# Kernel optimization log

Hardware: AMD Instinct MI355X
Metric: run time of the kernel (lower is better)

## Reference

```python
import jax, jax.numpy as jnp
import numpy as np

MASK_OUT_VALUE = -10000.0


def setup_inputs() -> dict:
    key = jax.random.key(0)
    k1, k2, k3 = jax.random.split(key, 3)
    B, H, S, D = 2, 16, 2048, 64
    query = jax.random.normal(k1, (B, H, S, D), dtype=jnp.float32)
    key_t = jax.random.normal(k2, (B, H, S, D), dtype=jnp.float32)
    value = jax.random.normal(k3, (B, H, S, D), dtype=jnp.float32)
    # causal mask: (1, 1, S, S), True where attention is allowed
    mask = jnp.tril(jnp.ones((S, S), dtype=bool))[None, None, :, :]
    return {"query": query, "key": key_t, "value": value, "mask": mask}


def reference(query, key, value, mask):
    # scores: (B, H, S, S)
    scale = 1.0 / jnp.sqrt(jnp.asarray(query.shape[-1], query.dtype))
    attn_scores = jnp.einsum("bhqd,bhkd->bhqk", query, key) * scale
    attn_scores = jnp.where(mask, attn_scores,
                            jnp.asarray(MASK_OUT_VALUE, attn_scores.dtype))
    attn_weights = jax.nn.softmax(attn_scores, axis=-1)
    # dropout is identity (p=0 / eval mode)
    attn_output = jnp.einsum("bhqk,bhkd->bhqd", attn_weights, value)
    return attn_output
```

## Files before the change

kernel.cpp:

```cpp
#include <hip/hip_runtime.h>
#include <math.h>


#define S_LEN   2048
#define D_HEAD  64
#define SCALE_L2E 0.18033688011112042f
#define FIXM    8.0f

using bf16x8 = __attribute__((ext_vector_type(8))) short;
using f32x4  = __attribute__((ext_vector_type(4))) float;
using uint4v = __attribute__((ext_vector_type(4))) unsigned int;

__device__ __forceinline__ unsigned int rnd_bf(float f) {
  return __float_as_uint(f) + 0x8000u;
}
__device__ __forceinline__ unsigned short f2bf(float f) {
  return (unsigned short)(rnd_bf(f) >> 16);
}

__device__ __forceinline__ void gl_lds16(const unsigned short* g, unsigned short* l) {
  __builtin_amdgcn_global_load_lds(
      (const __attribute__((address_space(1))) unsigned int*)g,
      (__attribute__((address_space(3))) unsigned int*)l, 16, 0, 0);
}

__device__ __forceinline__ unsigned int cvtpk_bf16(float lo, float hi) {
  unsigned int r;
  asm("v_cvt_pk_bf16_f32 %0, %1, %2" : "=v"(r) : "v"(lo), "v"(hi));
  return r;
}
__device__ __forceinline__ void swap32(unsigned int& a, unsigned int& b) {
  asm("v_permlane32_swap_b32 %0, %1" : "+v"(a), "+v"(b));
}
__device__ __forceinline__ void swap16(unsigned int& a, unsigned int& b) {
  asm("v_permlane16_swap_b32 %0, %1" : "+v"(a), "+v"(b));
}

template <int CTRL>
__device__ __forceinline__ float dppf(float x) {
  return __builtin_bit_cast(float,
      __builtin_amdgcn_update_dpp(0, __builtin_bit_cast(int, x), CTRL, 0xF, 0xF, false));
}
__device__ __forceinline__ float rowsum16(float x) {
  x += dppf<0xB1>(x);
  x += dppf<0x4E>(x);
  x += dppf<0x124>(x);
  x += dppf<0x128>(x);
  return x;
}

__global__ __launch_bounds__(256, 4)
void prep(const float* __restrict__ Kg, const float* __restrict__ Vg,
          unsigned short* __restrict__ Kb, unsigned short* __restrict__ Vt)
{
  __shared__ __align__(16) unsigned short Lt[64][72];
  const int j = blockIdx.x, t = threadIdx.x;
  const int bh = j >> 4, seg = j & 15;
  const size_t base = (size_t)bh * (S_LEN * D_HEAD) + (size_t)seg * 128 * D_HEAD;
#pragma unroll
  for (int i = 0; i < 8; ++i) {
    const size_t idx = base + i * 1024 + t * 4;
    const f32x4 v = *(const f32x4*)(Kg + idx);
    uint2 pk;
    pk.x = (rnd_bf(v[1]) & 0xFFFF0000u) | (rnd_bf(v[0]) >> 16);
    pk.y = (rnd_bf(v[3]) & 0xFFFF0000u) | (rnd_bf(v[2]) >> 16);
    *(uint2*)(Kb + idx) = pk;
  }
  for (int h = 0; h < 2; ++h) {
    const int s0 = seg * 128 + h * 64;
    __syncthreads();
#pragma unroll
    for (int pp = 0; pp < 4; ++pp) {
      const int r = t >> 2;
      const int d0 = (t & 3) * 4 + pp * 16;
      const f32x4 v = *(const f32x4*)(Vg + (size_t)bh * (S_LEN * D_HEAD)
                                         + (size_t)(s0 + r) * D_HEAD + d0);
#pragma unroll
      for (int e = 0; e < 4; ++e) Lt[d0 + e][r] = f2bf(v[e]);
    }
    __syncthreads();
#pragma unroll
    for (int q = 0; q < 2; ++q) {
      const int d = t >> 2, ch = (t & 3) + 4 * q;
      *(uint4*)(Vt + (size_t)(bh * 64 + d) * S_LEN + s0 + ch * 8) =
          *(const uint4*)&Lt[d][ch * 8];
    }
  }
}

__global__ __launch_bounds__(256, 2)
void fa(const float* __restrict__ Qg, const unsigned short* __restrict__ Kb,
        const unsigned short* __restrict__ Vt, float* __restrict__ Og)
{
  __shared__ unsigned short Ks[2][64][64];
  __shared__ unsigned short Vs[2][64][64];

  const int id = blockIdx.x;
  const int bh = id & 31;
  const int pr = id >> 5;

  const int t    = threadIdx.x;
  const int w    = t >> 6;
  const int lane = t & 63;
  const int c    = lane & 15;
  const int quad = lane >> 4;

  const float* __restrict__ Qb = Qg + (size_t)bh * (S_LEN * D_HEAD);
  float* __restrict__ Ob = Og + (size_t)bh * (S_LEN * D_HEAD);

  int fOff[4][2];
#pragma unroll
  for (int ci = 0; ci < 4; ++ci)
#pragma unroll
    for (int h = 0; h < 2; ++h)
      fOff[ci][h] = ((ci * 16 + c) << 6) + (((h * 4 + quad) ^ (c & 7)) << 3);

  const int rl = lane >> 3;
  const int jj = (lane & 7) ^ rl;
  auto stage = [&](int kt, int buf) {
#pragma unroll
    for (int n = 0; n < 2; ++n) {
      const int row = w * 16 + n * 8 + rl;
      gl_lds16(Kb + (((size_t)(bh * S_LEN + kt * 64 + row)) << 6) + jj * 8,
               &Ks[buf][w * 16 + n * 8][0]);
      gl_lds16(Vt + (((size_t)(bh * 64 + row)) << 11) + kt * 64 + jj * 8,
               &Vs[buf][w * 16 + n * 8][0]);
    }
  };

  bf16x8 qa[2];
  f32x4 oa[4];
  float ls;

  int tog = 0;
  stage(0, 0);

#pragma unroll 1
  for (int ph = 0; ph < 2; ++ph) {
    const int tr   = ph ? (31 - pr) : pr;
    const int row0 = tr * 64 + w * 16;

    {
      const float* qp = Qb + (size_t)(row0 + c) * D_HEAD + quad * 8;
#pragma unroll
      for (int h = 0; h < 2; ++h) {
        f32x4 a0 = *(const f32x4*)(qp + 32 * h);
        f32x4 a1 = *(const f32x4*)(qp + 32 * h + 4);
#pragma unroll
        for (int j = 0; j < 4; ++j) {
          qa[h][j]     = (short)f2bf(a0[j] * SCALE_L2E);
          qa[h][4 + j] = (short)f2bf(a1[j] * SCALE_L2E);
        }
      }
    }
#pragma unroll
    for (int i = 0; i < 4; ++i) oa[i] = (f32x4){0.f, 0.f, 0.f, 0.f};
    ls = 0.f;

#pragma unroll 1
    for (int kt = 0; kt <= tr; ++kt) {
      __syncthreads();
      const int nxt = tog ^ 1;
      if (kt < tr)            stage(kt + 1, nxt);
      else if (ph == 0)       stage(0, nxt);

      const unsigned short* ksc = &Ks[tog][0][0];
      const unsigned short* vsc = &Vs[tog][0][0];
      bf16x8 kf[4][2], vf[4][2];
#pragma unroll
      for (int ci = 0; ci < 4; ++ci)
#pragma unroll
        for (int h = 0; h < 2; ++h) {
          kf[ci][h] = *(const bf16x8*)(ksc + fOff[ci][h]);
          vf[ci][h] = *(const bf16x8*)(vsc + fOff[ci][h]);
        }

      __builtin_amdgcn_s_setprio(1);
      f32x4 sc[4];
#pragma unroll
      for (int ci = 0; ci < 4; ++ci) {
        f32x4 acc = (f32x4){-FIXM, -FIXM, -FIXM, -FIXM};
        acc = __builtin_amdgcn_mfma_f32_16x16x32_bf16(kf[ci][0], qa[0], acc, 0, 0, 0);
        acc = __builtin_amdgcn_mfma_f32_16x16x32_bf16(kf[ci][1], qa[1], acc, 0, 0, 0);
        sc[ci] = acc;
      }
      if (kt == tr) {
        const int grow = row0 + c;
#pragma unroll
        for (int ci = 0; ci < 4; ++ci)
#pragma unroll
          for (int r = 0; r < 4; ++r)
            if (kt * 64 + ci * 16 + quad * 4 + r > grow) sc[ci][r] = -1e30f;
      }
      unsigned int Wt[4][2];
#pragma unroll
      for (int ci = 0; ci < 4; ++ci) {
#pragma unroll
        for (int r = 0; r < 4; ++r)
          sc[ci][r] = __builtin_amdgcn_exp2f(sc[ci][r]);
        ls += (sc[ci][0] + sc[ci][1]) + (sc[ci][2] + sc[ci][3]);
        Wt[ci][0] = cvtpk_bf16(sc[ci][0], sc[ci][1]);
        Wt[ci][1] = cvtpk_bf16(sc[ci][2], sc[ci][3]);
      }
      unsigned int a00 = Wt[0][0], a02 = Wt[1][0]; swap32(a00, a02); swap16(a00, a02);
      unsigned int a01 = Wt[0][1], a03 = Wt[1][1]; swap32(a01, a03); swap16(a01, a03);
      unsigned int a10 = Wt[2][0], a12 = Wt[3][0]; swap32(a10, a12); swap16(a10, a12);
      unsigned int a11 = Wt[2][1], a13 = Wt[3][1]; swap32(a11, a13); swap16(a11, a13);
      const bf16x8 pa0 = __builtin_bit_cast(bf16x8, (uint4v){a00, a01, a02, a03});
      const bf16x8 pa1 = __builtin_bit_cast(bf16x8, (uint4v){a10, a11, a12, a13});

#pragma unroll
      for (int ci = 0; ci < 4; ++ci) {
        oa[ci] = __builtin_amdgcn_mfma_f32_16x16x32_bf16(pa0, vf[ci][0], oa[ci], 0, 0, 0);
        oa[ci] = __builtin_amdgcn_mfma_f32_16x16x32_bf16(pa1, vf[ci][1], oa[ci], 0, 0, 0);
      }
      __builtin_amdgcn_s_setprio(0);

      tog = nxt;
    }

    {
      float tot = ls;
      tot += __shfl_xor(tot, 16, 64);
      tot += __shfl_xor(tot, 32, 64);
      float inv[4];
#pragma unroll
      for (int r = 0; r < 4; ++r)
        inv[r] = 1.0f / __shfl(tot, quad * 4 + r, 64);
#pragma unroll
      for (int ci = 0; ci < 4; ++ci)
#pragma unroll
        for (int r = 0; r < 4; ++r)
          Ob[(size_t)(row0 + quad * 4 + r) * D_HEAD + ci * 16 + c] =
              oa[ci][r] * inv[r];
    }
  }
}

__global__ __launch_bounds__(256, 4)
void fa_fb(const float* __restrict__ Qg, const float* __restrict__ Kg,
           const float* __restrict__ Vg, float* __restrict__ Og)
{
  __shared__ __align__(16) unsigned short Ksh[64][72];
  __shared__ __align__(16) unsigned short Vsh[64][72];
  __shared__ __align__(16) unsigned short Psh[4][16][72];
  const int id = blockIdx.x;
  const int bh = id & 31;
  const int p  = id >> 5;
  const int t    = threadIdx.x;
  const int w    = t >> 6;
  const int lane = t & 63;
  const int c    = lane & 15;
  const int quad = lane >> 4;
  const size_t base = (size_t)bh * (S_LEN * D_HEAD);
  const float* __restrict__ Qb = Qg + base;
  const float* __restrict__ Kb = Kg + base;
  const float* __restrict__ Vb = Vg + base;
  float* __restrict__ Ob = Og + base;
  const int wv   = w & 1;
  const int row0 = (w >= 2) ? (S_LEN - 32 * (p + 1) + 16 * wv) : (32 * p + 16 * wv);
  const int ktdiag = row0 >> 6;
  const int ktmax  = (S_LEN - 1 - 32 * p) >> 6;
  bf16x8 qa[2];
  {
    const float* qp = Qb + (size_t)(row0 + c) * D_HEAD + quad * 8;
#pragma unroll
    for (int h = 0; h < 2; ++h) {
      f32x4 a0 = *(const f32x4*)(qp + 32 * h);
      f32x4 a1 = *(const f32x4*)(qp + 32 * h + 4);
#pragma unroll
      for (int j = 0; j < 4; ++j) {
        qa[h][j]     = (short)f2bf(a0[j] * SCALE_L2E);
        qa[h][4 + j] = (short)f2bf(a1[j] * SCALE_L2E);
      }
    }
  }
  f32x4 oa[4];
  float ls[4];
#pragma unroll
  for (int i = 0; i < 4; ++i) {
    oa[i] = (f32x4){0.f, 0.f, 0.f, 0.f};
    ls[i] = 0.f;
  }
  for (int kt = 0; kt <= ktmax; ++kt) {
    __syncthreads();
    {
      const int cp = t & 15;
      const int rg = t >> 4;
      const int col0 = cp * 4;
      const int sw = (cp >> 2) << 3;
#pragma unroll
      for (int i = 0; i < 4; ++i) {
        const int row = i * 16 + rg;
        const size_t goff = (size_t)(kt * 64 + row) * D_HEAD + col0;
        const f32x4 kv = *(const f32x4*)(Kb + goff);
        const f32x4 vv = *(const f32x4*)(Vb + goff);
        const unsigned int k01 = (rnd_bf(kv[1]) & 0xFFFF0000u) | (rnd_bf(kv[0]) >> 16);
        const unsigned int k23 = (rnd_bf(kv[3]) & 0xFFFF0000u) | (rnd_bf(kv[2]) >> 16);
        *(uint2*)&Ksh[row][col0] = make_uint2(k01, k23);
        const int kz = row ^ sw;
#pragma unroll
        for (int e = 0; e < 4; ++e)
          Vsh[col0 + e][kz] = f2bf(vv[e]);
      }
    }
    __syncthreads();
    if (kt <= ktdiag) {
      bf16x8 kf[4][2], vf[4][2];
#pragma unroll
      for (int ci = 0; ci < 4; ++ci) {
        kf[ci][0] = *(const bf16x8*)&Ksh[ci * 16 + c][quad * 8];
        kf[ci][1] = *(const bf16x8*)&Ksh[ci * 16 + c][32 + quad * 8];
        vf[ci][0] = *(const bf16x8*)&Vsh[ci * 16 + c][(quad ^ ci) * 8];
        vf[ci][1] = *(const bf16x8*)&Vsh[ci * 16 + c][32 + ((quad ^ ci) * 8)];
      }
      f32x4 sc[4];
#pragma unroll
      for (int ci = 0; ci < 4; ++ci) {
        f32x4 acc = (f32x4){-FIXM, -FIXM, -FIXM, -FIXM};
        acc = __builtin_amdgcn_mfma_f32_16x16x32_bf16(qa[0], kf[ci][0], acc, 0, 0, 0);
        acc = __builtin_amdgcn_mfma_f32_16x16x32_bf16(qa[1], kf[ci][1], acc, 0, 0, 0);
        sc[ci] = acc;
      }
      if (kt == ktdiag) {
#pragma unroll
        for (int ci = 0; ci < 4; ++ci) {
          const int gcol = kt * 64 + ci * 16 + c;
#pragma unroll
          for (int r = 0; r < 4; ++r)
            if (gcol > row0 + quad * 4 + r) sc[ci][r] = -1e30f;
        }
      }
#pragma unroll
      for (int ci = 0; ci < 4; ++ci)
#pragma unroll
        for (int r = 0; r < 4; ++r)
          sc[ci][r] = __builtin_amdgcn_exp2f(sc[ci][r]);
#pragma unroll
      for (int r = 0; r < 4; ++r)
        ls[r] += (sc[0][r] + sc[1][r]) + (sc[2][r] + sc[3][r]);
#pragma unroll
      for (int ci = 0; ci < 4; ++ci)
#pragma unroll
        for (int r = 0; r < 4; ++r) {
          const int prow = quad * 4 + r;
          Psh[w][prow][(ci * 16 + c) ^ ((prow >> 3) << 3)] = f2bf(sc[ci][r]);
        }
      const int px = (c >> 3) << 3;
      const bf16x8 pa0 = *(const bf16x8*)&Psh[w][c][(quad * 8) ^ px];
      const bf16x8 pa1 = *(const bf16x8*)&Psh[w][c][((32 + quad * 8)) ^ px];
#pragma unroll
      for (int ci = 0; ci < 4; ++ci) {
        oa[ci] = __builtin_amdgcn_mfma_f32_16x16x32_bf16(pa0, vf[ci][0], oa[ci], 0, 0, 0);
        oa[ci] = __builtin_amdgcn_mfma_f32_16x16x32_bf16(pa1, vf[ci][1], oa[ci], 0, 0, 0);
      }
    }
  }
  {
    float inv[4];
#pragma unroll
    for (int r = 0; r < 4; ++r) inv[r] = 1.0f / rowsum16(ls[r]);
#pragma unroll
    for (int ci = 0; ci < 4; ++ci)
#pragma unroll
      for (int r = 0; r < 4; ++r)
        Ob[(size_t)(row0 + quad * 4 + r) * D_HEAD + ci * 16 + c] = oa[ci][r] * inv[r];
  }
}

extern "C" void kernel_launch(void* const* d_in, const int* in_sizes, int n_in,
                              void* d_out, int out_size, void* d_ws, size_t ws_size,
                              hipStream_t stream) {
  (void)in_sizes; (void)n_in; (void)out_size;
  const float* Q = (const float*)d_in[0];
  const float* K = (const float*)d_in[1];
  const float* V = (const float*)d_in[2];
  float* O = (float*)d_out;
  const size_t NEED = 2ull * 32 * S_LEN * D_HEAD * 2;
  if (ws_size >= NEED) {
    unsigned short* Kb = (unsigned short*)d_ws;
    unsigned short* Vt = Kb + (size_t)32 * S_LEN * D_HEAD;
    prep<<<dim3(512), dim3(256), 0, stream>>>(K, V, Kb, Vt);
    fa<<<dim3(512), dim3(256), 0, stream>>>(Q, Kb, Vt, O);
  } else {
    fa_fb<<<dim3(1024), dim3(256), 0, stream>>>(Q, K, V, O);
  }
}
```

Before: 137.0 us.

## Split key tiles across two wave groups per block and merge partial outputs in LDS

```diff
diff --git a/kernel.cpp b/kernel.cpp
--- a/kernel.cpp
+++ b/kernel.cpp
@@ -88,19 +88,21 @@
   }
 }
 
-__global__ __launch_bounds__(256, 2)
+__global__ __launch_bounds__(512, 4)
 void fa(const float* __restrict__ Qg, const unsigned short* __restrict__ Kb,
         const unsigned short* __restrict__ Vt, float* __restrict__ Og)
 {
-  __shared__ unsigned short Ks[2][64][64];
-  __shared__ unsigned short Vs[2][64][64];
+  __shared__ unsigned short Ks[2][2][64][64];
+  __shared__ unsigned short Vs[2][2][64][64];
 
   const int id = blockIdx.x;
   const int bh = id & 31;
   const int pr = id >> 5;
 
   const int t    = threadIdx.x;
-  const int w    = t >> 6;
+  const int w8   = t >> 6;
+  const int g    = w8 >> 2;
+  const int wg   = w8 & 3;
   const int lane = t & 63;
   const int c    = lane & 15;
   const int quad = lane >> 4;
@@ -120,11 +122,11 @@
   auto stage = [&](int kt, int buf) {
 #pragma unroll
     for (int n = 0; n < 2; ++n) {
-      const int row = w * 16 + n * 8 + rl;
+      const int row = wg * 16 + n * 8 + rl;
       gl_lds16(Kb + (((size_t)(bh * S_LEN + kt * 64 + row)) << 6) + jj * 8,
-               &Ks[buf][w * 16 + n * 8][0]);
+               &Ks[g][buf][wg * 16 + n * 8][0]);
       gl_lds16(Vt + (((size_t)(bh * 64 + row)) << 11) + kt * 64 + jj * 8,
-               &Vs[buf][w * 16 + n * 8][0]);
+               &Vs[g][buf][wg * 16 + n * 8][0]);
     }
   };
 
@@ -132,13 +134,14 @@
   f32x4 oa[4];
   float ls;
 
-  int tog = 0;
-  stage(0, 0);
+  int slot = 0;
+  stage(g, 0);
 
 #pragma unroll 1
   for (int ph = 0; ph < 2; ++ph) {
-    const int tr   = ph ? (31 - pr) : pr;
-    const int row0 = tr * 64 + w * 16;
+    const int tr   = ph ? pr : (31 - pr);
+    const int row0 = tr * 64 + wg * 16;
+    const int hs   = (tr + 2) >> 1;
 
     {
       const float* qp = Qb + (size_t)(row0 + c) * D_HEAD + quad * 8;
@@ -158,69 +161,86 @@
     ls = 0.f;
 
 #pragma unroll 1
-    for (int kt = 0; kt <= tr; ++kt) {
+    for (int it = 0; it < hs; ++it, ++slot) {
+      const int kt  = 2 * it + g;
+      const int tog = slot & 1;
       __syncthreads();
-      const int nxt = tog ^ 1;
-      if (kt < tr)            stage(kt + 1, nxt);
-      else if (ph == 0)       stage(0, nxt);
-
-      const unsigned short* ksc = &Ks[tog][0][0];
-      const unsigned short* vsc = &Vs[tog][0][0];
-      bf16x8 kf[4][2], vf[4][2];
+      const int ktn = kt + 2;
+      if (ktn <= tr)
+        stage(ktn, tog ^ 1);
+      else if (ph == 0 && it == hs - 1 && g <= pr)
+        stage(g, tog ^ 1);
+
+      if (kt <= tr) {
+        const unsigned short* ksc = &Ks[g][tog][0][0];
+        const unsigned short* vsc = &Vs[g][tog][0][0];
+        bf16x8 kf[4][2], vf[4][2];
+#pragma unroll
+        for (int ci = 0; ci < 4; ++ci)
+#pragma unroll
+          for (int h = 0; h < 2; ++h) {
+            kf[ci][h] = *(const bf16x8*)(ksc + fOff[ci][h]);
+            vf[ci][h] = *(const bf16x8*)(vsc + fOff[ci][h]);
+          }
+
+        __builtin_amdgcn_s_setprio(1);
+        f32x4 sc[4];
+#pragma unroll
+        for (int ci = 0; ci < 4; ++ci) {
+          f32x4 acc = (f32x4){-FIXM, -FIXM, -FIXM, -FIXM};
+          acc = __builtin_amdgcn_mfma_f32_16x16x32_bf16(kf[ci][0], qa[0], acc, 0, 0, 0);
+          acc = __builtin_amdgcn_mfma_f32_16x16x32_bf16(kf[ci][1], qa[1], acc, 0, 0, 0);
+          sc[ci] = acc;
+        }
+        if (kt == tr) {
+          const int grow = row0 + c;
+#pragma unroll
+          for (int ci = 0; ci < 4; ++ci)
+#pragma unroll
+            for (int r = 0; r < 4; ++r)
+              if (kt * 64 + ci * 16 + quad * 4 + r > grow) sc[ci][r] = -1e30f;
+        }
+        unsigned int Wt[4][2];
+#pragma unroll
+        for (int ci = 0; ci < 4; ++ci) {
+#pragma unroll
+          for (int r = 0; r < 4; ++r)
+            sc[ci][r] = __builtin_amdgcn_exp2f(sc[ci][r]);
+          ls += (sc[ci][0] + sc[ci][1]) + (sc[ci][2] + sc[ci][3]);
+          Wt[ci][0] = cvtpk_bf16(sc[ci][0], sc[ci][1]);
+          Wt[ci][1] = cvtpk_bf16(sc[ci][2], sc[ci][3]);
+        }
+        unsigned int a00 = Wt[0][0], a02 = Wt[1][0]; swap32(a00, a02); swap16(a00, a02);
+        unsigned int a01 = Wt[0][1], a03 = Wt[1][1]; swap32(a01, a03); swap16(a01, a03);
+        unsigned int a10 = Wt[2][0], a12 = Wt[3][0]; swap32(a10, a12); swap16(a10, a12);
+        unsigned int a11 = Wt[2][1], a13 = Wt[3][1]; swap32(a11, a13); swap16(a11, a13);
+        const bf16x8 pa0 = __builtin_bit_cast(bf16x8, (uint4v){a00, a01, a02, a03});
+        const bf16x8 pa1 = __builtin_bit_cast(bf16x8, (uint4v){a10, a11, a12, a13});
+
+#pragma unroll
+        for (int ci = 0; ci < 4; ++ci) {
+          oa[ci] = __builtin_amdgcn_mfma_f32_16x16x32_bf16(pa0, vf[ci][0], oa[ci], 0, 0, 0);
+          oa[ci] = __builtin_amdgcn_mfma_f32_16x16x32_bf16(pa1, vf[ci][1], oa[ci], 0, 0, 0);
+        }
+        __builtin_amdgcn_s_setprio(0);
+      }
+    }
+
+    const int fp = (slot & 1) ^ 1;
+    __syncthreads();
+    if (g == 1) {
+      float* exo = (float*)&Vs[wg >> 1][fp][0][0] + (wg & 1) * 1024;
 #pragma unroll
       for (int ci = 0; ci < 4; ++ci)
 #pragma unroll
-        for (int h = 0; h < 2; ++h) {
-          kf[ci][h] = *(const bf16x8*)(ksc + fOff[ci][h]);
-          vf[ci][h] = *(const bf16x8*)(vsc + fOff[ci][h]);
-        }
-
-      __builtin_amdgcn_s_setprio(1);
-      f32x4 sc[4];
-#pragma unroll
-      for (int ci = 0; ci < 4; ++ci) {
-        f32x4 acc = (f32x4){-FIXM, -FIXM, -FIXM, -FIXM};
-        acc = __builtin_amdgcn_mfma_f32_16x16x32_bf16(kf[ci][0], qa[0], acc, 0, 0, 0);
-        acc = __builtin_amdgcn_mfma_f32_16x16x32_bf16(kf[ci][1], qa[1], acc, 0, 0, 0);
-        sc[ci] = acc;
-      }
-      if (kt == tr) {
-        const int grow = row0 + c;
-#pragma unroll
-        for (int ci = 0; ci < 4; ++ci)
-#pragma unroll
-          for (int r = 0; r < 4; ++r)
-            if (kt * 64 + ci * 16 + quad * 4 + r > grow) sc[ci][r] = -1e30f;
-      }
-      unsigned int Wt[4][2];
-#pragma unroll
-      for (int ci = 0; ci < 4; ++ci) {
-#pragma unroll
         for (int r = 0; r < 4; ++r)
-          sc[ci][r] = __builtin_amdgcn_exp2f(sc[ci][r]);
-        ls += (sc[ci][0] + sc[ci][1]) + (sc[ci][2] + sc[ci][3]);
-        Wt[ci][0] = cvtpk_bf16(sc[ci][0], sc[ci][1]);
-        Wt[ci][1] = cvtpk_bf16(sc[ci][2], sc[ci][3]);
-      }
-      unsigned int a00 = Wt[0][0], a02 = Wt[1][0]; swap32(a00, a02); swap16(a00, a02);
-      unsigned int a01 = Wt[0][1], a03 = Wt[1][1]; swap32(a01, a03); swap16(a01, a03);
-      unsigned int a10 = Wt[2][0], a12 = Wt[3][0]; swap32(a10, a12); swap16(a10, a12);
-      unsigned int a11 = Wt[2][1], a13 = Wt[3][1]; swap32(a11, a13); swap16(a11, a13);
-      const bf16x8 pa0 = __builtin_bit_cast(bf16x8, (uint4v){a00, a01, a02, a03});
-      const bf16x8 pa1 = __builtin_bit_cast(bf16x8, (uint4v){a10, a11, a12, a13});
-
-#pragma unroll
-      for (int ci = 0; ci < 4; ++ci) {
-        oa[ci] = __builtin_amdgcn_mfma_f32_16x16x32_bf16(pa0, vf[ci][0], oa[ci], 0, 0, 0);
-        oa[ci] = __builtin_amdgcn_mfma_f32_16x16x32_bf16(pa1, vf[ci][1], oa[ci], 0, 0, 0);
-      }
-      __builtin_amdgcn_s_setprio(0);
-
-      tog = nxt;
-    }
-
-    {
-      float tot = ls;
+          exo[(ci * 4 + r) * 64 + lane] = oa[ci][r];
+      ((float*)&Ks[0][fp][0][0])[wg * 64 + lane] = ls;
+    }
+    __syncthreads();
+    if (g == 0) {
+      const float* exo = (const float*)&Vs[wg >> 1][fp][0][0] + (wg & 1) * 1024;
+      float tot = ls + ((const float*)&Ks[0][fp][0][0])[wg * 64 + lane];
       tot += __shfl_xor(tot, 16, 64);
       tot += __shfl_xor(tot, 32, 64);
       float inv[4];
@@ -230,9 +250,10 @@
 #pragma unroll
       for (int ci = 0; ci < 4; ++ci)
 #pragma unroll
-        for (int r = 0; r < 4; ++r)
-          Ob[(size_t)(row0 + quad * 4 + r) * D_HEAD + ci * 16 + c] =
-              oa[ci][r] * inv[r];
+        for (int r = 0; r < 4; ++r) {
+          const float ov = oa[ci][r] + exo[(ci * 4 + r) * 64 + lane];
+          Ob[(size_t)(row0 + quad * 4 + r) * D_HEAD + ci * 16 + c] = ov * inv[r];
+        }
     }
   }
 }
@@ -381,7 +402,7 @@
     unsigned short* Kb = (unsigned short*)d_ws;
     unsigned short* Vt = Kb + (size_t)32 * S_LEN * D_HEAD;
     prep<<<dim3(512), dim3(256), 0, stream>>>(K, V, Kb, Vt);
-    fa<<<dim3(512), dim3(256), 0, stream>>>(Q, Kb, Vt, O);
+    fa<<<dim3(512), dim3(512), 0, stream>>>(Q, Kb, Vt, O);
   } else {
     fa_fb<<<dim3(1024), dim3(256), 0, stream>>>(Q, K, V, O);
   }
```

After: 135.5 us. Within noise of the previous version (-1.1%).

## Stage two K/V tiles per barrier to halve synchronization count

Applied to the files above, without the earlier changes.

```diff
diff --git a/kernel.cpp b/kernel.cpp
--- a/kernel.cpp
+++ b/kernel.cpp
@@ -92,8 +92,8 @@
 void fa(const float* __restrict__ Qg, const unsigned short* __restrict__ Kb,
         const unsigned short* __restrict__ Vt, float* __restrict__ Og)
 {
-  __shared__ unsigned short Ks[2][64][64];
-  __shared__ unsigned short Vs[2][64][64];
+  __shared__ unsigned short Ks[2][2][64][64];
+  __shared__ unsigned short Vs[2][2][64][64];
 
   const int id = blockIdx.x;
   const int bh = id & 31;
@@ -108,6 +108,8 @@
   const float* __restrict__ Qb = Qg + (size_t)bh * (S_LEN * D_HEAD);
   float* __restrict__ Ob = Og + (size_t)bh * (S_LEN * D_HEAD);
 
+  const int tr0 = pr, tr1 = 31 - pr;
+
   int fOff[4][2];
 #pragma unroll
   for (int ci = 0; ci < 4; ++ci)
@@ -117,28 +119,34 @@
 
   const int rl = lane >> 3;
   const int jj = (lane & 7) ^ rl;
-  auto stage = [&](int kt, int buf) {
+  auto stage1 = [&](int kt, int buf, int sub) {
 #pragma unroll
     for (int n = 0; n < 2; ++n) {
       const int row = w * 16 + n * 8 + rl;
       gl_lds16(Kb + (((size_t)(bh * S_LEN + kt * 64 + row)) << 6) + jj * 8,
-               &Ks[buf][w * 16 + n * 8][0]);
+               &Ks[buf][sub][w * 16 + n * 8][0]);
       gl_lds16(Vt + (((size_t)(bh * 64 + row)) << 11) + kt * 64 + jj * 8,
-               &Vs[buf][w * 16 + n * 8][0]);
-    }
+               &Vs[buf][sub][w * 16 + n * 8][0]);
+    }
+  };
+  auto stage_pair = [&](int it, int tr, int buf) {
+    const int k0 = 2 * it;
+    stage1(k0, buf, 0);
+    if (k0 + 1 <= tr) stage1(k0 + 1, buf, 1);
   };
 
   bf16x8 qa[2];
   f32x4 oa[4];
   float ls;
 
-  int tog = 0;
-  stage(0, 0);
+  int buf = 0;
+  stage_pair(0, tr0, 0);
 
 #pragma unroll 1
   for (int ph = 0; ph < 2; ++ph) {
-    const int tr   = ph ? (31 - pr) : pr;
-    const int row0 = tr * 64 + w * 16;
+    const int tr    = ph ? tr1 : tr0;
+    const int row0  = tr * 64 + w * 16;
+    const int iters = (tr + 2) >> 1;
 
     {
       const float* qp = Qb + (size_t)(row0 + c) * D_HEAD + quad * 8;
@@ -158,65 +166,69 @@
     ls = 0.f;
 
 #pragma unroll 1
-    for (int kt = 0; kt <= tr; ++kt) {
+    for (int it = 0; it < iters; ++it) {
       __syncthreads();
-      const int nxt = tog ^ 1;
-      if (kt < tr)            stage(kt + 1, nxt);
-      else if (ph == 0)       stage(0, nxt);
-
-      const unsigned short* ksc = &Ks[tog][0][0];
-      const unsigned short* vsc = &Vs[tog][0][0];
-      bf16x8 kf[4][2], vf[4][2];
-#pragma unroll
-      for (int ci = 0; ci < 4; ++ci)
-#pragma unroll
-        for (int h = 0; h < 2; ++h) {
-          kf[ci][h] = *(const bf16x8*)(ksc + fOff[ci][h]);
-          vf[ci][h] = *(const bf16x8*)(vsc + fOff[ci][h]);
+      if (it + 1 < iters)  stage_pair(it + 1, tr, buf ^ 1);
+      else if (ph == 0)    stage_pair(0, tr1, buf ^ 1);
+
+#pragma unroll
+      for (int s = 0; s < 2; ++s) {
+        const int kt = 2 * it + s;
+        if (kt <= tr) {
+          const unsigned short* ksc = &Ks[buf][s][0][0];
+          const unsigned short* vsc = &Vs[buf][s][0][0];
+          bf16x8 kf[4][2], vf[4][2];
+#pragma unroll
+          for (int ci = 0; ci < 4; ++ci)
+#pragma unroll
+            for (int h = 0; h < 2; ++h) {
+              kf[ci][h] = *(const bf16x8*)(ksc + fOff[ci][h]);
+              vf[ci][h] = *(const bf16x8*)(vsc + fOff[ci][h]);
+            }
+
+          __builtin_amdgcn_s_setprio(1);
+          f32x4 sc[4];
+#pragma unroll
+          for (int ci = 0; ci < 4; ++ci) {
+            f32x4 acc = (f32x4){-FIXM, -FIXM, -FIXM, -FIXM};
+            acc = __builtin_amdgcn_mfma_f32_16x16x32_bf16(kf[ci][0], qa[0], acc, 0, 0, 0);
+            acc = __builtin_amdgcn_mfma_f32_16x16x32_bf16(kf[ci][1], qa[1], acc, 0, 0, 0);
+            sc[ci] = acc;
+          }
+          if (kt == tr) {
+            const int grow = row0 + c;
+#pragma unroll
+            for (int ci = 0; ci < 4; ++ci)
+#pragma unroll
+              for (int r = 0; r < 4; ++r)
+                if (kt * 64 + ci * 16 + quad * 4 + r > grow) sc[ci][r] = -1e30f;
+          }
+          unsigned int Wt[4][2];
+#pragma unroll
+          for (int ci = 0; ci < 4; ++ci) {
+#pragma unroll
+            for (int r = 0; r < 4; ++r)
+              sc[ci][r] = __builtin_amdgcn_exp2f(sc[ci][r]);
+            ls += (sc[ci][0] + sc[ci][1]) + (sc[ci][2] + sc[ci][3]);
+            Wt[ci][0] = cvtpk_bf16(sc[ci][0], sc[ci][1]);
+            Wt[ci][1] = cvtpk_bf16(sc[ci][2], sc[ci][3]);
+          }
+          unsigned int a00 = Wt[0][0], a02 = Wt[1][0]; swap32(a00, a02); swap16(a00, a02);
+          unsigned int a01 = Wt[0][1], a03 = Wt[1][1]; swap32(a01, a03); swap16(a01, a03);
+          unsigned int a10 = Wt[2][0], a12 = Wt[3][0]; swap32(a10, a12); swap16(a10, a12);
+          unsigned int a11 = Wt[2][1], a13 = Wt[3][1]; swap32(a11, a13); swap16(a11, a13);
+          const bf16x8 pa0 = __builtin_bit_cast(bf16x8, (uint4v){a00, a01, a02, a03});
+          const bf16x8 pa1 = __builtin_bit_cast(bf16x8, (uint4v){a10, a11, a12, a13});
+
+#pragma unroll
+          for (int ci = 0; ci < 4; ++ci) {
+            oa[ci] = __builtin_amdgcn_mfma_f32_16x16x32_bf16(pa0, vf[ci][0], oa[ci], 0, 0, 0);
+            oa[ci] = __builtin_amdgcn_mfma_f32_16x16x32_bf16(pa1, vf[ci][1], oa[ci], 0, 0, 0);
+          }
+          __builtin_amdgcn_s_setprio(0);
         }
-
-      __builtin_amdgcn_s_setprio(1);
-      f32x4 sc[4];
-#pragma unroll
-      for (int ci = 0; ci < 4; ++ci) {
-        f32x4 acc = (f32x4){-FIXM, -FIXM, -FIXM, -FIXM};
-        acc = __builtin_amdgcn_mfma_f32_16x16x32_bf16(kf[ci][0], qa[0], acc, 0, 0, 0);
-        acc = __builtin_amdgcn_mfma_f32_16x16x32_bf16(kf[ci][1], qa[1], acc, 0, 0, 0);
-        sc[ci] = acc;
-      }
-      if (kt == tr) {
-        const int grow = row0 + c;
-#pragma unroll
-        for (int ci = 0; ci < 4; ++ci)
-#pragma unroll
-          for (int r = 0; r < 4; ++r)
-            if (kt * 64 + ci * 16 + quad * 4 + r > grow) sc[ci][r] = -1e30f;
-      }
-      unsigned int Wt[4][2];
-#pragma unroll
-      for (int ci = 0; ci < 4; ++ci) {
-#pragma unroll
-        for (int r = 0; r < 4; ++r)
-          sc[ci][r] = __builtin_amdgcn_exp2f(sc[ci][r]);
-        ls += (sc[ci][0] + sc[ci][1]) + (sc[ci][2] + sc[ci][3]);
-        Wt[ci][0] = cvtpk_bf16(sc[ci][0], sc[ci][1]);
-        Wt[ci][1] = cvtpk_bf16(sc[ci][2], sc[ci][3]);
-      }
-      unsigned int a00 = Wt[0][0], a02 = Wt[1][0]; swap32(a00, a02); swap16(a00, a02);
-      unsigned int a01 = Wt[0][1], a03 = Wt[1][1]; swap32(a01, a03); swap16(a01, a03);
-      unsigned int a10 = Wt[2][0], a12 = Wt[3][0]; swap32(a10, a12); swap16(a10, a12);
-      unsigned int a11 = Wt[2][1], a13 = Wt[3][1]; swap32(a11, a13); swap16(a11, a13);
-      const bf16x8 pa0 = __builtin_bit_cast(bf16x8, (uint4v){a00, a01, a02, a03});
-      const bf16x8 pa1 = __builtin_bit_cast(bf16x8, (uint4v){a10, a11, a12, a13});
-
-#pragma unroll
-      for (int ci = 0; ci < 4; ++ci) {
-        oa[ci] = __builtin_amdgcn_mfma_f32_16x16x32_bf16(pa0, vf[ci][0], oa[ci], 0, 0, 0);
-        oa[ci] = __builtin_amdgcn_mfma_f32_16x16x32_bf16(pa1, vf[ci][1], oa[ci], 0, 0, 0);
-      }
-      __builtin_amdgcn_s_setprio(0);
-
-      tog = nxt;
+      }
+      buf ^= 1;
     }
 
     {
```

Result: faster. 131.5 us (-4.0%).

## Load K/V fragments directly from global into registers, drop LDS staging

Applied to the files above, without the earlier changes.

```diff
diff --git a/kernel.cpp b/kernel.cpp
--- a/kernel.cpp
+++ b/kernel.cpp
@@ -16,12 +16,6 @@
 }
 __device__ __forceinline__ unsigned short f2bf(float f) {
   return (unsigned short)(rnd_bf(f) >> 16);
-}
-
-__device__ __forceinline__ void gl_lds16(const unsigned short* g, unsigned short* l) {
-  __builtin_amdgcn_global_load_lds(
-      (const __attribute__((address_space(1))) unsigned int*)g,
-      (__attribute__((address_space(3))) unsigned int*)l, 16, 0, 0);
 }
 
 __device__ __forceinline__ unsigned int cvtpk_bf16(float lo, float hi) {
@@ -92,9 +86,6 @@
 void fa(const float* __restrict__ Qg, const unsigned short* __restrict__ Kb,
         const unsigned short* __restrict__ Vt, float* __restrict__ Og)
 {
-  __shared__ unsigned short Ks[2][64][64];
-  __shared__ unsigned short Vs[2][64][64];
-
   const int id = blockIdx.x;
   const int bh = id & 31;
   const int pr = id >> 5;
@@ -106,133 +97,142 @@
   const int quad = lane >> 4;
 
   const float* __restrict__ Qb = Qg + (size_t)bh * (S_LEN * D_HEAD);
+  const unsigned short* __restrict__ Kbb = Kb + (size_t)bh * (S_LEN * D_HEAD);
+  const unsigned short* __restrict__ Vtb = Vt + (size_t)bh * (D_HEAD * S_LEN);
   float* __restrict__ Ob = Og + (size_t)bh * (S_LEN * D_HEAD);
 
-  int fOff[4][2];
+  const int trA = pr, trB = 31 - pr;
+  const int rowA = trA * 64 + w * 16, rowB = trB * 64 + w * 16;
+
+  int kOff[4][2], vOff[4][2];
 #pragma unroll
   for (int ci = 0; ci < 4; ++ci)
 #pragma unroll
-    for (int h = 0; h < 2; ++h)
-      fOff[ci][h] = ((ci * 16 + c) << 6) + (((h * 4 + quad) ^ (c & 7)) << 3);
-
-  const int rl = lane >> 3;
-  const int jj = (lane & 7) ^ rl;
-  auto stage = [&](int kt, int buf) {
-#pragma unroll
-    for (int n = 0; n < 2; ++n) {
-      const int row = w * 16 + n * 8 + rl;
-      gl_lds16(Kb + (((size_t)(bh * S_LEN + kt * 64 + row)) << 6) + jj * 8,
-               &Ks[buf][w * 16 + n * 8][0]);
-      gl_lds16(Vt + (((size_t)(bh * 64 + row)) << 11) + kt * 64 + jj * 8,
-               &Vs[buf][w * 16 + n * 8][0]);
-    }
-  };
-
-  bf16x8 qa[2];
-  f32x4 oa[4];
-  float ls;
-
-  int tog = 0;
-  stage(0, 0);
-
-#pragma unroll 1
-  for (int ph = 0; ph < 2; ++ph) {
-    const int tr   = ph ? (31 - pr) : pr;
-    const int row0 = tr * 64 + w * 16;
-
-    {
-      const float* qp = Qb + (size_t)(row0 + c) * D_HEAD + quad * 8;
+    for (int h = 0; h < 2; ++h) {
+      kOff[ci][h] = (ci * 16 + c) * 64   + h * 32 + quad * 8;
+      vOff[ci][h] = (ci * 16 + c) * 2048 + h * 32 + quad * 8;
+    }
+
+  bf16x8 ones;
+#pragma unroll
+  for (int j = 0; j < 8; ++j) ones[j] = (short)0x3F80;
+
+  bf16x8 qa0[2], qa1[2];
+  {
+#pragma unroll
+    for (int ph = 0; ph < 2; ++ph) {
+      const float* qp = Qb + (size_t)((ph ? rowB : rowA) + c) * D_HEAD + quad * 8;
 #pragma unroll
       for (int h = 0; h < 2; ++h) {
         f32x4 a0 = *(const f32x4*)(qp + 32 * h);
         f32x4 a1 = *(const f32x4*)(qp + 32 * h + 4);
 #pragma unroll
         for (int j = 0; j < 4; ++j) {
-          qa[h][j]     = (short)f2bf(a0[j] * SCALE_L2E);
-          qa[h][4 + j] = (short)f2bf(a1[j] * SCALE_L2E);
+          if (ph) { qa1[h][j] = (short)f2bf(a0[j] * SCALE_L2E);
+                    qa1[h][4 + j] = (short)f2bf(a1[j] * SCALE_L2E); }
+          else    { qa0[h][j] = (short)f2bf(a0[j] * SCALE_L2E);
+                    qa0[h][4 + j] = (short)f2bf(a1[j] * SCALE_L2E); }
         }
       }
     }
-#pragma unroll
-    for (int i = 0; i < 4; ++i) oa[i] = (f32x4){0.f, 0.f, 0.f, 0.f};
-    ls = 0.f;
-
-#pragma unroll 1
-    for (int kt = 0; kt <= tr; ++kt) {
-      __syncthreads();
-      const int nxt = tog ^ 1;
-      if (kt < tr)            stage(kt + 1, nxt);
-      else if (ph == 0)       stage(0, nxt);
-
-      const unsigned short* ksc = &Ks[tog][0][0];
-      const unsigned short* vsc = &Vs[tog][0][0];
-      bf16x8 kf[4][2], vf[4][2];
+  }
+
+  f32x4 oa[4];
+  f32x4 lacc;
+#pragma unroll
+  for (int i = 0; i < 4; ++i) oa[i] = (f32x4){0.f, 0.f, 0.f, 0.f};
+  lacc = (f32x4){0.f, 0.f, 0.f, 0.f};
+
+  auto loadKV = [&](int i, bf16x8 (&kf)[4][2], bf16x8 (&vf)[4][2]) {
+    const int kt = (i <= trA) ? i : (i - trA - 1);
+    const unsigned short* kp = Kbb + kt * (64 * 64);
+    const unsigned short* vp = Vtb + kt * 64;
+#pragma unroll
+    for (int ci = 0; ci < 4; ++ci)
+#pragma unroll
+      for (int h = 0; h < 2; ++h) {
+        kf[ci][h] = *(const bf16x8*)(kp + kOff[ci][h]);
+        vf[ci][h] = *(const bf16x8*)(vp + vOff[ci][h]);
+      }
+  };
+
+  auto smpack = [&](f32x4* sc, bf16x8& p0, bf16x8& p1) {
+    unsigned int Wt[4][2];
+#pragma unroll
+    for (int ci = 0; ci < 4; ++ci) {
+#pragma unroll
+      for (int r = 0; r < 4; ++r)
+        sc[ci][r] = __builtin_amdgcn_exp2f(sc[ci][r]);
+      Wt[ci][0] = cvtpk_bf16(sc[ci][0], sc[ci][1]);
+      Wt[ci][1] = cvtpk_bf16(sc[ci][2], sc[ci][3]);
+    }
+    unsigned int a00 = Wt[0][0], a02 = Wt[1][0]; swap32(a00, a02); swap16(a00, a02);
+    unsigned int a01 = Wt[0][1], a03 = Wt[1][1]; swap32(a01, a03); swap16(a01, a03);
+    unsigned int a10 = Wt[2][0], a12 = Wt[3][0]; swap32(a10, a12); swap16(a10, a12);
+    unsigned int a11 = Wt[2][1], a13 = Wt[3][1]; swap32(a11, a13); swap16(a11, a13);
+    p0 = __builtin_bit_cast(bf16x8, (uint4v){a00, a01, a02, a03});
+    p1 = __builtin_bit_cast(bf16x8, (uint4v){a10, a11, a12, a13});
+  };
+
+  auto doTile = [&](int kt, int tr, int row0, const bf16x8 (&qaf)[2],
+                    bf16x8 (&kf)[4][2], bf16x8 (&vf)[4][2]) {
+    __builtin_amdgcn_s_setprio(1);
+    f32x4 sc[4];
+#pragma unroll
+    for (int ci = 0; ci < 4; ++ci) {
+      f32x4 acc = (f32x4){-FIXM, -FIXM, -FIXM, -FIXM};
+      acc = __builtin_amdgcn_mfma_f32_16x16x32_bf16(kf[ci][0], qaf[0], acc, 0, 0, 0);
+      acc = __builtin_amdgcn_mfma_f32_16x16x32_bf16(kf[ci][1], qaf[1], acc, 0, 0, 0);
+      sc[ci] = acc;
+    }
+    if (kt == tr) {
+      const int grow = row0 + c;
 #pragma unroll
       for (int ci = 0; ci < 4; ++ci)
 #pragma unroll
-        for (int h = 0; h < 2; ++h) {
-          kf[ci][h] = *(const bf16x8*)(ksc + fOff[ci][h]);
-          vf[ci][h] = *(const bf16x8*)(vsc + fOff[ci][h]);
-        }
-
-      __builtin_amdgcn_s_setprio(1);
-      f32x4 sc[4];
-#pragma unroll
-      for (int ci = 0; ci < 4; ++ci) {
-        f32x4 acc = (f32x4){-FIXM, -FIXM, -FIXM, -FIXM};
-        acc = __builtin_amdgcn_mfma_f32_16x16x32_bf16(kf[ci][0], qa[0], acc, 0, 0, 0);
-        acc = __builtin_amdgcn_mfma_f32_16x16x32_bf16(kf[ci][1], qa[1], acc, 0, 0, 0);
-        sc[ci] = acc;
-      }
-      if (kt == tr) {
-        const int grow = row0 + c;
-#pragma unroll
-        for (int ci = 0; ci < 4; ++ci)
-#pragma unroll
-          for (int r = 0; r < 4; ++r)
-            if (kt * 64 + ci * 16 + quad * 4 + r > grow) sc[ci][r] = -1e30f;
-      }
-      unsigned int Wt[4][2];
-#pragma unroll
-      for (int ci = 0; ci < 4; ++ci) {
-#pragma unroll
         for (int r = 0; r < 4; ++r)
-          sc[ci][r] = __builtin_amdgcn_exp2f(sc[ci][r]);
-        ls += (sc[ci][0] + sc[ci][1]) + (sc[ci][2] + sc[ci][3]);
-        Wt[ci][0] = cvtpk_bf16(sc[ci][0], sc[ci][1]);
-        Wt[ci][1] = cvtpk_bf16(sc[ci][2], sc[ci][3]);
-      }
-      unsigned int a00 = Wt[0][0], a02 = Wt[1][0]; swap32(a00, a02); swap16(a00, a02);
-      unsigned int a01 = Wt[0][1], a03 = Wt[1][1]; swap32(a01, a03); swap16(a01, a03);
-      unsigned int a10 = Wt[2][0], a12 = Wt[3][0]; swap32(a10, a12); swap16(a10, a12);
-      unsigned int a11 = Wt[2][1], a13 = Wt[3][1]; swap32(a11, a13); swap16(a11, a13);
-      const bf16x8 pa0 = __builtin_bit_cast(bf16x8, (uint4v){a00, a01, a02, a03});
-      const bf16x8 pa1 = __builtin_bit_cast(bf16x8, (uint4v){a10, a11, a12, a13});
-
-#pragma unroll
-      for (int ci = 0; ci < 4; ++ci) {
-        oa[ci] = __builtin_amdgcn_mfma_f32_16x16x32_bf16(pa0, vf[ci][0], oa[ci], 0, 0, 0);
-        oa[ci] = __builtin_amdgcn_mfma_f32_16x16x32_bf16(pa1, vf[ci][1], oa[ci], 0, 0, 0);
-      }
-      __builtin_amdgcn_s_setprio(0);
-
-      tog = nxt;
-    }
-
-    {
-      float tot = ls;
-      tot += __shfl_xor(tot, 16, 64);
-      tot += __shfl_xor(tot, 32, 64);
+          if (kt * 64 + ci * 16 + quad * 4 + r > grow) sc[ci][r] = -1e30f;
+    }
+    bf16x8 p0, p1;
+    smpack(sc, p0, p1);
+#pragma unroll
+    for (int ci = 0; ci < 4; ++ci) {
+      oa[ci] = __builtin_amdgcn_mfma_f32_16x16x32_bf16(p0, vf[ci][0], oa[ci], 0, 0, 0);
+      oa[ci] = __builtin_amdgcn_mfma_f32_16x16x32_bf16(p1, vf[ci][1], oa[ci], 0, 0, 0);
+    }
+    lacc = __builtin_amdgcn_mfma_f32_16x16x32_bf16(p0, ones, lacc, 0, 0, 0);
+    lacc = __builtin_amdgcn_mfma_f32_16x16x32_bf16(p1, ones, lacc, 0, 0, 0);
+    __builtin_amdgcn_s_setprio(0);
+    if (kt == tr) {
       float inv[4];
 #pragma unroll
-      for (int r = 0; r < 4; ++r)
-        inv[r] = 1.0f / __shfl(tot, quad * 4 + r, 64);
+      for (int r = 0; r < 4; ++r) inv[r] = 1.0f / lacc[r];
 #pragma unroll
       for (int ci = 0; ci < 4; ++ci)
 #pragma unroll
         for (int r = 0; r < 4; ++r)
           Ob[(size_t)(row0 + quad * 4 + r) * D_HEAD + ci * 16 + c] =
               oa[ci][r] * inv[r];
+#pragma unroll
+      for (int i2 = 0; i2 < 4; ++i2) oa[i2] = (f32x4){0.f, 0.f, 0.f, 0.f};
+      lacc = (f32x4){0.f, 0.f, 0.f, 0.f};
+    }
+  };
+
+  auto compute = [&](int i, bf16x8 (&kf)[4][2], bf16x8 (&vf)[4][2]) {
+    if (i <= trA) doTile(i, trA, rowA, qa0, kf, vf);
+    else          doTile(i - trA - 1, trB, rowB, qa1, kf, vf);
+  };
+
+  bf16x8 kfA[4][2], vfA[4][2], kfB[4][2], vfB[4][2];
+  loadKV(0, kfA, vfA);
+#pragma unroll 1
+  for (int i = 0; i < 33; i += 2) {
+    if (i + 1 < 33) loadKV(i + 1, kfB, vfB);
+    compute(i, kfA, vfA);
+    if (i + 1 < 33) {
+      if (i + 2 < 33) loadKV(i + 2, kfA, vfA);
+      compute(i + 1, kfB, vfB);
     }
   }
 }
```

After: 222.0 us. 62.0% more time.
